# Kernel tuning notes

Measured on AMD Instinct MI355X. Metric: run time of the kernel, lower is better.

The kernel has to match this reference:

```python
import jax, jax.numpy as jnp
import numpy as np

B, S, H, NH, L = 2, 1024, 512, 8, 4
HD = H // NH
MLP = 4 * H
OUT = 128
SPARSITY = 0.8
EPS = 1e-5


def _pos_encoding(seq_len, d_model):
    pos = jnp.arange(seq_len, dtype=jnp.float32)[:, None]                     # [S,1]
    div = jnp.exp(jnp.arange(0, d_model, 2, dtype=jnp.float32) * (-np.log(10000.0) / d_model))
    ang = pos * div                                                            # [S,D/2]
    pe = jnp.stack([jnp.sin(ang), jnp.cos(ang)], axis=-1).reshape(seq_len, d_model)
    return pe[None]                                                            # [1,S,D]


def _layer_norm(x, g, b):
    m = jnp.mean(x, axis=-1, keepdims=True)
    v = jnp.mean(jnp.square(x - m), axis=-1, keepdims=True)
    return (x - m) * jax.lax.rsqrt(v + EPS) * g + b


def setup_inputs() -> dict:
    key = jax.random.key(0)
    ks = iter(jax.random.split(key, 16))
    w = lambda k, shp: jax.random.normal(k, shp, dtype=jnp.float32) * 0.02
    inp = {
        "x": jax.random.normal(next(ks), (B, S), dtype=jnp.float32),
        "in_w": w(next(ks), (1, H)), "in_b": jnp.zeros((H,), jnp.float32),
        "ln1_g": jnp.ones((L, H), jnp.float32), "ln1_b": jnp.zeros((L, H), jnp.float32),
        "qw": w(next(ks), (L, H, H)), "qb": jnp.zeros((L, H), jnp.float32),
        "kw": w(next(ks), (L, H, H)), "kb": jnp.zeros((L, H), jnp.float32),
        "vw": w(next(ks), (L, H, H)), "vb": jnp.zeros((L, H), jnp.float32),
        "ow": w(next(ks), (L, H, H)), "ob": jnp.zeros((L, H), jnp.float32),
        "ln2_g": jnp.ones((L, H), jnp.float32), "ln2_b": jnp.zeros((L, H), jnp.float32),
        "w1": w(next(ks), (L, H, MLP)), "b1": jnp.zeros((L, MLP), jnp.float32),
        "w2": w(next(ks), (L, MLP, H)), "b2": jnp.zeros((L, H), jnp.float32),
        "fn_g": jnp.ones((H,), jnp.float32), "fn_b": jnp.zeros((H,), jnp.float32),
        "out_w": w(next(ks), (H, OUT)), "out_b": jnp.zeros((OUT,), jnp.float32),
    }
    return inp


def _forward(x, in_w, in_b, ln1_g, ln1_b, qw, qb, kw, kb, vw, vb, ow, ob,
             ln2_g, ln2_b, w1, b1, w2, b2, fn_g, fn_b, out_w, out_b):
    seq_len = x.shape[1]
    k_top = max(1, int(seq_len * (1.0 - SPARSITY)))  # static
    scale = HD ** -0.5

    h = x[..., None] @ in_w + in_b                    # [B,S,H] (input_proj on [B,S,1])
    h = h + _pos_encoding(seq_len, H)

    layer_params = (ln1_g, ln1_b, qw, qb, kw, kb, vw, vb, ow, ob,
                    ln2_g, ln2_b, w1, b1, w2, b2)

    def block(h, p):
        (g1, bb1, Wq, bq, Wk, bk, Wv, bv, Wo, bo, g2, bb2, W1, B1, W2, B2) = p
        n = _layer_norm(h, g1, bb1)
        # project and split heads: [B,S,H] -> [B,NH,S,HD]
        def heads(W, b):
            y = n @ W + b
            return y.reshape(B, seq_len, NH, HD).transpose(0, 2, 1, 3)
        q, k, v = heads(Wq, bq), heads(Wk, bk), heads(Wv, bv)
        scores = jnp.einsum('bhqd,bhkd->bhqk', q, k) * scale
        # top-k sparsification: keep entries >= k-th largest per row (-inf elsewhere)
        kth = jax.lax.top_k(scores, k_top)[0][..., -1:]
        sparse = jnp.where(scores >= kth, scores, -jnp.inf)
        attn = jax.nn.softmax(sparse, axis=-1)
        o = jnp.einsum('bhqk,bhkd->bhqd', attn, v)
        o = o.transpose(0, 2, 1, 3).reshape(B, seq_len, H)
        h = h + (o @ Wo + bo)
        m = _layer_norm(h, g2, bb2)
        m = jax.nn.gelu(m @ W1 + B1, approximate=False) @ W2 + B2
        return h + m, attn

    h, attn_stack = jax.lax.scan(block, h, layer_params)
    out = _layer_norm(h, fn_g, fn_b) @ out_w + out_b  # [B,S,OUT]
    return out, attn_stack                            # attn_stack: [L,B,NH,S,S]


def reference(x, in_w, in_b, ln1_g, ln1_b, qw, qb, kw, kb, vw, vb, ow, ob,
              ln2_g, ln2_b, w1, b1, w2, b2, fn_g, fn_b, out_w, out_b):
    return _forward(x, in_w, in_b, ln1_g, ln1_b, qw, qb, kw, kb, vw, vb, ow, ob,
                    ln2_g, ln2_b, w1, b1, w2, b2, fn_g, fn_b, out_w, out_b)
```

## Files before the change

### kernel.cpp

```cpp
#include <hip/hip_runtime.h>
#include <math.h>

#define DEVINL __device__ __forceinline__

constexpr int S_   = 1024;
constexpr int H_   = 512;
constexpr int NH_  = 8;
constexpr int L_   = 4;
constexpr int HD_  = 64;
constexpr int MLP_ = 2048;
constexpr int OUT_ = 128;
constexpr int B_   = 2;
constexpr int BS_  = 2048;
constexpr int KTOP_ = 204;

typedef __bf16 bf16x8 __attribute__((ext_vector_type(8)));
typedef float f32x4 __attribute__((ext_vector_type(4)));

DEVINL unsigned short f2b(float f) {
  unsigned int u = __float_as_uint(f);
  unsigned int r = (u + 0x7fffu + ((u >> 16) & 1u)) >> 16;
  return (unsigned short)r;
}

DEVINL void gload16(const unsigned short* g, unsigned short* l) {
  __builtin_amdgcn_global_load_lds(
      (const __attribute__((address_space(1))) unsigned int*)g,
      (__attribute__((address_space(3))) unsigned int*)l,
      16, 0, 0);
}

__global__ __launch_bounds__(256) void transpose_conv_kernel(
    const float* __restrict__ src, unsigned short* __restrict__ dst, int R, int C)
{
  __shared__ float tile[32][33];
  const size_t base = (size_t)blockIdx.z * R * C;
  src += base; dst += base;
  const int c0 = blockIdx.x * 32;
  const int r0 = blockIdx.y * 32;
  const int tx = threadIdx.x & 31;
  const int ty = threadIdx.x >> 5;
#pragma unroll
  for (int j = 0; j < 4; j++)
    tile[ty + j * 8][tx] = src[(size_t)(r0 + ty + j * 8) * C + c0 + tx];
  __syncthreads();
#pragma unroll
  for (int j = 0; j < 4; j++)
    dst[(size_t)(c0 + ty + j * 8) * R + r0 + tx] = f2b(tile[tx][ty + j * 8]);
}

__global__ __launch_bounds__(256) void transpose_qkvo_kernel(
    const float* __restrict__ qw, const float* __restrict__ kw,
    const float* __restrict__ vw, const float* __restrict__ ow,
    unsigned short* __restrict__ qkv, unsigned short* __restrict__ ot)
{
  __shared__ float tile[32][33];
  const int z = blockIdx.z;
  const int which = z >> 2, l = z & 3;
  const float* src = (which == 0 ? qw : which == 1 ? kw : which == 2 ? vw : ow)
                     + (size_t)l * 512 * 512;
  unsigned short* dst = (which < 3)
      ? (qkv + (size_t)l * 1536 * 512 + (size_t)which * 512 * 512)
      : (ot + (size_t)l * 512 * 512);
  const int c0 = blockIdx.x * 32;
  const int r0 = blockIdx.y * 32;
  const int tx = threadIdx.x & 31;
  const int ty = threadIdx.x >> 5;
#pragma unroll
  for (int j = 0; j < 4; j++)
    tile[ty + j * 8][tx] = src[(size_t)(r0 + ty + j * 8) * 512 + c0 + tx];
  __syncthreads();
#pragma unroll
  for (int j = 0; j < 4; j++)
    dst[(size_t)(c0 + ty + j * 8) * 512 + r0 + tx] = f2b(tile[tx][ty + j * 8]);
}

__global__ __launch_bounds__(128) void input_pe_kernel(
    const float* __restrict__ x, const float* __restrict__ in_w,
    const float* __restrict__ in_b, float* __restrict__ h)
{
  const int row = blockIdx.x;
  const int s = row & (S_ - 1);
  const int c = threadIdx.x * 4;
  const float xv = x[row];
  const float4 wv = *(const float4*)(in_w + c);
  const float4 bv = *(const float4*)(in_b + c);
  const float* wp = (const float*)&wv;
  const float* bp = (const float*)&bv;
  float o[4];
#pragma unroll
  for (int j = 0; j < 4; j++) {
    const int cc = c + j;
    const float di = expf(-(float)(cc & ~1) * (9.210340371976184f / 512.0f));
    const float ang = (float)s * di;
    const float pe = (cc & 1) ? cosf(ang) : sinf(ang);
    o[j] = xv * wp[j] + bp[j] + pe;
  }
  *(float4*)(h + (size_t)row * H_ + c) = make_float4(o[0], o[1], o[2], o[3]);
}

__global__ __launch_bounds__(128) void ln_kernel(
    const float* __restrict__ hin, const float* __restrict__ g,
    const float* __restrict__ b, unsigned short* __restrict__ nout)
{
  const int row = blockIdx.x;
  const int t = threadIdx.x;
  const int wid = t >> 6, ln_ = t & 63;
  __shared__ float red[2];
  float4 v = ((const float4*)(hin + (size_t)row * H_))[t];
  float sm = v.x + v.y + v.z + v.w;
#pragma unroll
  for (int m = 1; m < 64; m <<= 1) sm += __shfl_xor(sm, m);
  if (ln_ == 0) red[wid] = sm;
  __syncthreads();
  const float mean = (red[0] + red[1]) * (1.0f / 512.0f);
  __syncthreads();
  const float dx = v.x - mean, dy = v.y - mean, dz = v.z - mean, dw = v.w - mean;
  float ss = dx * dx + dy * dy + dz * dz + dw * dw;
#pragma unroll
  for (int m = 1; m < 64; m <<= 1) ss += __shfl_xor(ss, m);
  if (ln_ == 0) red[wid] = ss;
  __syncthreads();
  const float var = (red[0] + red[1]) * (1.0f / 512.0f);
  const float rs = rsqrtf(var + 1e-5f);
  const float4 gv = ((const float4*)g)[t];
  const float4 bv = ((const float4*)b)[t];
  ushort4 o;
  o.x = f2b(dx * rs * gv.x + bv.x);
  o.y = f2b(dy * rs * gv.y + bv.y);
  o.z = f2b(dz * rs * gv.z + bv.z);
  o.w = f2b(dw * rs * gv.w + bv.w);
  ((ushort4*)(nout + (size_t)row * H_))[t] = o;
}

template <int EPI>
__global__ __launch_bounds__(256, 2) void gemm_kernel(
    const unsigned short* __restrict__ A, const unsigned short* __restrict__ Bt,
    const float* __restrict__ bias, void* __restrict__ Cout,
    int M, int N, int Klen, int Kstride,
    const float* __restrict__ bias2, const float* __restrict__ bias3,
    void* __restrict__ C2, void* __restrict__ C3)
{
  __shared__ unsigned short Alds[128 * 32];
  __shared__ unsigned short Blds[128 * 32];
  const int tid = threadIdx.x;
  const int w = tid >> 6, lane = tid & 63, lr = lane & 15, lg = lane >> 4;
  const int m0 = blockIdx.x * 128, n0 = blockIdx.y * 128;
  const int wm = (w >> 1) * 64, wn = (w & 1) * 64;

  A  += (size_t)blockIdx.z * Klen;
  Bt += (size_t)blockIdx.z * Klen;

  const int srow = w * 32 + (lane >> 2);
  const int scol = (lane & 3) * 8;
  const unsigned short* Ag0 = A + (size_t)(m0 + srow) * Kstride + scol;
  const unsigned short* Ag1 = A + (size_t)(m0 + srow + 16) * Kstride + scol;
  const unsigned short* Bg0 = Bt + (size_t)(n0 + srow) * Kstride + scol;
  const unsigned short* Bg1 = Bt + (size_t)(n0 + srow + 16) * Kstride + scol;
  unsigned short* Al0 = Alds + (w * 32) * 32;
  unsigned short* Al1 = Alds + (w * 32 + 16) * 32;
  unsigned short* Bl0 = Blds + (w * 32) * 32;
  unsigned short* Bl1 = Blds + (w * 32 + 16) * 32;

  const f32x4 zero4 = {0.f, 0.f, 0.f, 0.f};
  f32x4 acc[4][4];
#pragma unroll
  for (int i = 0; i < 4; i++)
#pragma unroll
    for (int j = 0; j < 4; j++) acc[i][j] = zero4;

  for (int kt = 0; kt < Klen; kt += 32) {
    __syncthreads();
    gload16(Ag0 + kt, Al0);
    gload16(Ag1 + kt, Al1);
    gload16(Bg0 + kt, Bl0);
    gload16(Bg1 + kt, Bl1);
    __syncthreads();
    bf16x8 af[4], bfr[4];
#pragma unroll
    for (int mi = 0; mi < 4; mi++)
      af[mi] = *(const bf16x8*)(Alds + (wm + mi * 16 + lr) * 32 + lg * 8);
#pragma unroll
    for (int ni = 0; ni < 4; ni++)
      bfr[ni] = *(const bf16x8*)(Blds + (wn + ni * 16 + lr) * 32 + lg * 8);
#pragma unroll
    for (int mi = 0; mi < 4; mi++)
#pragma unroll
      for (int ni = 0; ni < 4; ni++)
        acc[mi][ni] = __builtin_amdgcn_mfma_f32_16x16x32_bf16(af[mi], bfr[ni], acc[mi][ni], 0, 0, 0);
  }

#pragma unroll
  for (int mi = 0; mi < 4; mi++) {
#pragma unroll
    for (int ni = 0; ni < 4; ni++) {
      const int col = n0 + wn + ni * 16 + lr;
      if constexpr (EPI == 5) {
        if (col < 512) {
          const float bs = bias[col];
#pragma unroll
          for (int r = 0; r < 4; r++) {
            const int row = m0 + wm + mi * 16 + lg * 4 + r;
            ((unsigned short*)Cout)[(size_t)row * 512 + col] =
                f2b((acc[mi][ni][r] + bs) * 0.125f);
          }
        } else if (col < 1024) {
          const float bs = bias2[col - 512];
#pragma unroll
          for (int r = 0; r < 4; r++) {
            const int row = m0 + wm + mi * 16 + lg * 4 + r;
            ((unsigned short*)C2)[(size_t)row * 512 + (col - 512)] =
                f2b(acc[mi][ni][r] + bs);
          }
        } else {
          const float bs = bias3[col - 1024];
          const int row0_ = m0 + wm + mi * 16 + lg * 4;
          const int bb = row0_ >> 10, ssi = row0_ & 1023;
          ushort4 pk;
          pk.x = f2b(acc[mi][ni][0] + bs);
          pk.y = f2b(acc[mi][ni][1] + bs);
          pk.z = f2b(acc[mi][ni][2] + bs);
          pk.w = f2b(acc[mi][ni][3] + bs);
          *(ushort4*)((unsigned short*)C3 + ((size_t)(bb * 512 + (col - 1024))) * 1024 + ssi) = pk;
        }
      } else if constexpr (EPI == 6) {
        const float bs = (blockIdx.z == 0) ? bias[col] : 0.f;
#pragma unroll
        for (int r = 0; r < 4; r++) {
          const int row = m0 + wm + mi * 16 + lg * 4 + r;
          atomicAdd(&((float*)Cout)[(size_t)row * N + col], acc[mi][ni][r] + bs);
        }
      } else {
        const float bs = bias[col];
#pragma unroll
        for (int r = 0; r < 4; r++) {
          const int row = m0 + wm + mi * 16 + lg * 4 + r;
          float val = acc[mi][ni][r] + bs;
          const size_t idx = (size_t)row * N + col;
          if constexpr (EPI == 2) {
            val = 0.5f * val * (1.0f + erff(val * 0.7071067811865475f));
            ((unsigned short*)Cout)[idx] = f2b(val);
          } else {
            ((float*)Cout)[idx] = val;
          }
        }
      }
    }
  }
}

__global__ __launch_bounds__(256, 2) void attn_fused_kernel(
    const unsigned short* __restrict__ qbf, const unsigned short* __restrict__ kbf,
    const unsigned short* __restrict__ vt, float* __restrict__ attnL,
    unsigned short* __restrict__ obf)
{
  constexpr int LDF = 1032;
  __shared__ float sc[16 * LDF];
  const int mblk = blockIdx.x, bnh = blockIdx.y;
  const int b = bnh >> 3, nh = bnh & 7;
  const int tid = threadIdx.x, w = tid >> 6, lane = tid & 63;
  const int lr = lane & 15, lg = lane >> 4;
  const int row0 = mblk * 16;

  const unsigned short* qbase = qbf + ((size_t)(b * S_ + row0)) * H_ + nh * HD_;
  const unsigned short* kbase = kbf + (size_t)(b * S_) * H_ + nh * HD_;

  const f32x4 zero4 = {0.f, 0.f, 0.f, 0.f};

  {
    f32x4 acc[16];
#pragma unroll
    for (int kt = 0; kt < 16; kt++) acc[kt] = zero4;
    bf16x8 qf[2];
    qf[0] = *(const bf16x8*)(qbase + (size_t)lr * H_ + lg * 8);
    qf[1] = *(const bf16x8*)(qbase + (size_t)lr * H_ + 32 + lg * 8);
    const int kw0 = w * 256;
#pragma unroll
    for (int kt = 0; kt < 16; kt++) {
      const unsigned short* kp = kbase + (size_t)(kw0 + kt * 16 + lr) * H_ + lg * 8;
      const bf16x8 kf0 = *(const bf16x8*)(kp);
      const bf16x8 kf1 = *(const bf16x8*)(kp + 32);
      acc[kt] = __builtin_amdgcn_mfma_f32_16x16x32_bf16(kf0, qf[0], acc[kt], 0, 0, 0);
      acc[kt] = __builtin_amdgcn_mfma_f32_16x16x32_bf16(kf1, qf[1], acc[kt], 0, 0, 0);
    }
#pragma unroll
    for (int kt = 0; kt < 16; kt++)
      *(f32x4*)(sc + (size_t)lr * LDF + kw0 + kt * 16 + lg * 4) = acc[kt];
  }
  __syncthreads();

#pragma unroll 1
  for (int rr = 0; rr < 4; rr++) {
    const int row = w * 4 + rr;
    float* rowp = sc + (size_t)row * LDF;
    float v[16];
#pragma unroll
    for (int j = 0; j < 8; j++) {
      const float2 t2 = *(const float2*)(rowp + 2 * lane + j * 128);
      v[2 * j] = t2.x; v[2 * j + 1] = t2.y;
    }
    unsigned int keys[16];
#pragma unroll
    for (int j = 0; j < 16; j++) {
      const unsigned int u = __float_as_uint(v[j]);
      keys[j] = (u & 0x80000000u) ? ~u : (u | 0x80000000u);
    }
    unsigned int prefix = 0u;
#pragma unroll 1
    for (int bit = 31; bit >= 0; bit--) {
      const unsigned int cand = prefix | (1u << bit);
      int cnt = 0;
#pragma unroll
      for (int j = 0; j < 16; j++)
        cnt += (int)__popcll(__ballot(keys[j] >= cand));
      if (cnt >= KTOP_) prefix = cand;
    }
    const unsigned int fb = (prefix & 0x80000000u) ? (prefix & 0x7fffffffu) : ~prefix;
    const float thresh = __uint_as_float(fb);

    float mx = v[0];
#pragma unroll
    for (int j = 1; j < 16; j++) mx = fmaxf(mx, v[j]);
#pragma unroll
    for (int m = 1; m < 64; m <<= 1) mx = fmaxf(mx, __shfl_xor(mx, m));
    float p[16];
    float ssum = 0.f;
#pragma unroll
    for (int j = 0; j < 16; j++) {
      const float e = expf(v[j] - mx);
      p[j] = (v[j] >= thresh) ? e : 0.f;
      ssum += p[j];
    }
#pragma unroll
    for (int m = 1; m < 64; m <<= 1) ssum += __shfl_xor(ssum, m);
    const float inv = 1.0f / ssum;
    float* outrow = attnL + (size_t)bnh * S_ * S_ + (size_t)(row0 + row) * S_;
    unsigned short* prow = (unsigned short*)rowp;
#pragma unroll
    for (int j = 0; j < 8; j++) {
      const float p0 = p[2 * j] * inv, p1 = p[2 * j + 1] * inv;
      *(float2*)(outrow + 2 * lane + j * 128) = make_float2(p0, p1);
      const unsigned int pk = ((unsigned int)f2b(p1) << 16) | (unsigned int)f2b(p0);
      *(unsigned int*)(prow + 2 * lane + j * 128) = pk;
    }
  }
  __syncthreads();

  const unsigned short* vb = vt + (size_t)(b * 512 + nh * HD_) * S_;
  f32x4 oacc[4];
#pragma unroll
  for (int ni = 0; ni < 4; ni++) oacc[ni] = zero4;
  const unsigned short* scu = (const unsigned short*)sc;
#pragma unroll
  for (int ks = 0; ks < 8; ks++) {
    const int k0 = w * 256 + ks * 32;
    const bf16x8 pf = *(const bf16x8*)(scu + (size_t)lr * (2 * LDF) + k0 + lg * 8);
    bf16x8 vfr[4];
#pragma unroll
    for (int ni = 0; ni < 4; ni++)
      vfr[ni] = *(const bf16x8*)(vb + (size_t)(ni * 16 + lr) * S_ + k0 + lg * 8);
#pragma unroll
    for (int ni = 0; ni < 4; ni++)
      oacc[ni] = __builtin_amdgcn_mfma_f32_16x16x32_bf16(pf, vfr[ni], oacc[ni], 0, 0, 0);
  }
  __syncthreads();
  float* red = sc + w * 1024;
#pragma unroll
  for (int ni = 0; ni < 4; ni++)
#pragma unroll
    for (int r = 0; r < 4; r++)
      red[(lg * 4 + r) * 64 + ni * 16 + lr] = oacc[ni][r];
  __syncthreads();
  {
    const int orow = tid >> 4, oc0 = (tid & 15) * 4;
    const float* rp = sc + orow * 64 + oc0;
    float4 s0 = *(const float4*)rp;
#pragma unroll
    for (int ww = 1; ww < 4; ww++) {
      const float4 a = *(const float4*)(rp + ww * 1024);
      s0.x += a.x; s0.y += a.y; s0.z += a.z; s0.w += a.w;
    }
    ushort4 o1;
    o1.x = f2b(s0.x); o1.y = f2b(s0.y); o1.z = f2b(s0.z); o1.w = f2b(s0.w);
    unsigned short* dst = obf + (size_t)(b * S_ + row0 + orow) * H_ + nh * HD_ + oc0;
    *(ushort4*)dst = o1;
  }
}

extern "C" void kernel_launch(void* const* d_in, const int* in_sizes, int n_in,
                              void* d_out, int out_size, void* d_ws, size_t ws_size,
                              hipStream_t stream)
{
  (void)in_sizes; (void)n_in; (void)out_size; (void)ws_size;
  const float* x     = (const float*)d_in[0];
  const float* in_w  = (const float*)d_in[1];
  const float* in_b  = (const float*)d_in[2];
  const float* ln1_g = (const float*)d_in[3];
  const float* ln1_b = (const float*)d_in[4];
  const float* qw    = (const float*)d_in[5];
  const float* qbias = (const float*)d_in[6];
  const float* kw    = (const float*)d_in[7];
  const float* kbias = (const float*)d_in[8];
  const float* vw    = (const float*)d_in[9];
  const float* vbias = (const float*)d_in[10];
  const float* ow    = (const float*)d_in[11];
  const float* obias = (const float*)d_in[12];
  const float* ln2_g = (const float*)d_in[13];
  const float* ln2_b = (const float*)d_in[14];
  const float* w1    = (const float*)d_in[15];
  const float* b1    = (const float*)d_in[16];
  const float* w2    = (const float*)d_in[17];
  const float* b2    = (const float*)d_in[18];
  const float* fn_g  = (const float*)d_in[19];
  const float* fn_b  = (const float*)d_in[20];
  const float* out_w = (const float*)d_in[21];
  const float* out_b = (const float*)d_in[22];

  char* ws = (char*)d_ws;
  size_t off = 0;
  auto alloc = [&](size_t bytes) -> void* {
    void* p = ws + off;
    off += (bytes + 255) & ~(size_t)255;
    return p;
  };
  float* h             = (float*)alloc((size_t)BS_ * H_ * 4);
  unsigned short* Wqkvt = (unsigned short*)alloc((size_t)L_ * 1536 * H_ * 2);
  unsigned short* Wot  = (unsigned short*)alloc((size_t)L_ * H_ * H_ * 2);
  unsigned short* W1t  = (unsigned short*)alloc((size_t)L_ * MLP_ * H_ * 2);
  unsigned short* W2t  = (unsigned short*)alloc((size_t)L_ * H_ * MLP_ * 2);
  unsigned short* OWt  = (unsigned short*)alloc((size_t)OUT_ * H_ * 2);
  unsigned short* nbf  = (unsigned short*)alloc((size_t)BS_ * H_ * 2);
  unsigned short* qbf  = (unsigned short*)alloc((size_t)BS_ * H_ * 2);
  unsigned short* kbf  = (unsigned short*)alloc((size_t)BS_ * H_ * 2);
  unsigned short* vtb  = (unsigned short*)alloc((size_t)B_ * 512 * S_ * 2);
  unsigned short* obf  = (unsigned short*)alloc((size_t)BS_ * H_ * 2);
  unsigned short* tbf  = (unsigned short*)alloc((size_t)BS_ * MLP_ * 2);

  float* attn_base = (float*)d_out + (size_t)BS_ * OUT_;

  const dim3 tb(256);
  transpose_qkvo_kernel<<<dim3(16, 16, 16), tb, 0, stream>>>(qw, kw, vw, ow, Wqkvt, Wot);
  transpose_conv_kernel<<<dim3(64, 16, 4), tb, 0, stream>>>(w1, W1t, H_, MLP_);
  transpose_conv_kernel<<<dim3(16, 64, 4), tb, 0, stream>>>(w2, W2t, MLP_, H_);
  transpose_conv_kernel<<<dim3(4, 16, 1),  tb, 0, stream>>>(out_w, OWt, H_, OUT_);

  input_pe_kernel<<<dim3(BS_), dim3(128), 0, stream>>>(x, in_w, in_b, h);

  for (int l = 0; l < L_; l++) {
    float* attnL = attn_base + (size_t)l * 16 * S_ * S_;
    ln_kernel<<<dim3(BS_), dim3(128), 0, stream>>>(h, ln1_g + l * H_, ln1_b + l * H_, nbf);
    gemm_kernel<5><<<dim3(16, 12), tb, 0, stream>>>(
        nbf, Wqkvt + (size_t)l * 1536 * H_, qbias + l * H_, qbf, BS_, 1536, H_, H_,
        kbias + l * H_, vbias + l * H_, kbf, vtb);
    attn_fused_kernel<<<dim3(64, 16), tb, 0, stream>>>(qbf, kbf, vtb, attnL, obf);
    gemm_kernel<6><<<dim3(16, 4, 2), tb, 0, stream>>>(
        obf, Wot + (size_t)l * H_ * H_, obias + l * H_, h, BS_, H_, 256, H_,
        nullptr, nullptr, nullptr, nullptr);
    ln_kernel<<<dim3(BS_), dim3(128), 0, stream>>>(h, ln2_g + l * H_, ln2_b + l * H_, nbf);
    gemm_kernel<2><<<dim3(16, 16), tb, 0, stream>>>(
        nbf, W1t + (size_t)l * MLP_ * H_, b1 + l * MLP_, tbf, BS_, MLP_, H_, H_,
        nullptr, nullptr, nullptr, nullptr);
    gemm_kernel<6><<<dim3(16, 4, 4), tb, 0, stream>>>(
        tbf, W2t + (size_t)l * H_ * MLP_, b2 + l * H_, h, BS_, H_, 512, MLP_,
        nullptr, nullptr, nullptr, nullptr);
  }

  ln_kernel<<<dim3(BS_), dim3(128), 0, stream>>>(h, fn_g, fn_b, nbf);
  gemm_kernel<3><<<dim3(16, 1), tb, 0, stream>>>(
      nbf, OWt, out_b, d_out, BS_, OUT_, H_, H_,
      nullptr, nullptr, nullptr, nullptr);
}
```

Measured before the change: 1.037 ms.

## Double-buffer GEMM LDS tiles and merge prep kernels into one launch

The GEMM main loop now uses two LDS buffers, so the global-to-LDS load of the next K tile is issued before the MFMAs on the current tile, and each iteration needs one barrier instead of two. The four weight transpose/convert kernels and the input projection plus positional-encoding kernel are merged into a single prep launch that dispatches by block index. This targets load latency exposed inside the GEMM loop and per-launch overhead in setup. Double buffering doubles GEMM LDS use, which may reduce occupancy under launch_bounds(256,2).

New measurement: 1.035 ms. About the same (-0.2%).

```diff
diff --git a/kernel.cpp b/kernel.cpp
--- a/kernel.cpp
+++ b/kernel.cpp
@@ -30,16 +30,68 @@
       16, 0, 0);
 }
 
-__global__ __launch_bounds__(256) void transpose_conv_kernel(
-    const float* __restrict__ src, unsigned short* __restrict__ dst, int R, int C)
+__global__ __launch_bounds__(256) void prep_kernel(
+    const float* __restrict__ qw, const float* __restrict__ kw,
+    const float* __restrict__ vw, const float* __restrict__ ow,
+    const float* __restrict__ w1, const float* __restrict__ w2,
+    const float* __restrict__ outw,
+    const float* __restrict__ x, const float* __restrict__ in_w,
+    const float* __restrict__ in_b,
+    unsigned short* __restrict__ Wqkvt, unsigned short* __restrict__ Wot,
+    unsigned short* __restrict__ W1t, unsigned short* __restrict__ W2t,
+    unsigned short* __restrict__ OWt, float* __restrict__ h)
 {
+  const int bid = blockIdx.x;
+  if (bid >= 12352) {
+    const int idx = bid - 12352;
+    const int row = idx * 2 + (threadIdx.x >> 7);
+    const int s = row & (S_ - 1);
+    const int c = (threadIdx.x & 127) * 4;
+    const float xv = x[row];
+    const float4 wv = *(const float4*)(in_w + c);
+    const float4 bv = *(const float4*)(in_b + c);
+    const float* wp = (const float*)&wv;
+    const float* bp = (const float*)&bv;
+    float o[4];
+#pragma unroll
+    for (int j = 0; j < 4; j++) {
+      const int cc = c + j;
+      const float di = expf(-(float)(cc & ~1) * (9.210340371976184f / 512.0f));
+      const float ang = (float)s * di;
+      const float pe = (cc & 1) ? cosf(ang) : sinf(ang);
+      o[j] = xv * wp[j] + bp[j] + pe;
+    }
+    *(float4*)(h + (size_t)row * H_ + c) = make_float4(o[0], o[1], o[2], o[3]);
+    return;
+  }
+  const float* src; unsigned short* dst; int R, C, cx, ry;
+  if (bid < 4096) {
+    const int z = bid >> 8, rem = bid & 255;
+    const int which = z >> 2, l = z & 3;
+    src = (which == 0 ? qw : which == 1 ? kw : which == 2 ? vw : ow)
+          + (size_t)l * 512 * 512;
+    dst = (which < 3)
+        ? (Wqkvt + (size_t)l * 1536 * 512 + (size_t)which * 512 * 512)
+        : (Wot + (size_t)l * 512 * 512);
+    R = 512; C = 512; cx = rem & 15; ry = rem >> 4;
+  } else if (bid < 8192) {
+    const int idx = bid - 4096, z = idx >> 10, rem = idx & 1023;
+    src = w1 + (size_t)z * 512 * 2048;
+    dst = W1t + (size_t)z * 2048 * 512;
+    R = 512; C = 2048; cx = rem & 63; ry = rem >> 6;
+  } else if (bid < 12288) {
+    const int idx = bid - 8192, z = idx >> 10, rem = idx & 1023;
+    src = w2 + (size_t)z * 2048 * 512;
+    dst = W2t + (size_t)z * 512 * 2048;
+    R = 2048; C = 512; cx = rem & 15; ry = rem >> 4;
+  } else {
+    const int idx = bid - 12288;
+    src = outw; dst = OWt;
+    R = 512; C = 128; cx = idx & 3; ry = idx >> 2;
+  }
   __shared__ float tile[32][33];
-  const size_t base = (size_t)blockIdx.z * R * C;
-  src += base; dst += base;
-  const int c0 = blockIdx.x * 32;
-  const int r0 = blockIdx.y * 32;
-  const int tx = threadIdx.x & 31;
-  const int ty = threadIdx.x >> 5;
+  const int c0 = cx * 32, r0 = ry * 32;
+  const int tx = threadIdx.x & 31, ty = threadIdx.x >> 5;
 #pragma unroll
   for (int j = 0; j < 4; j++)
     tile[ty + j * 8][tx] = src[(size_t)(r0 + ty + j * 8) * C + c0 + tx];
@@ -47,56 +99,6 @@
 #pragma unroll
   for (int j = 0; j < 4; j++)
     dst[(size_t)(c0 + ty + j * 8) * R + r0 + tx] = f2b(tile[tx][ty + j * 8]);
-}
-
-__global__ __launch_bounds__(256) void transpose_qkvo_kernel(
-    const float* __restrict__ qw, const float* __restrict__ kw,
-    const float* __restrict__ vw, const float* __restrict__ ow,
-    unsigned short* __restrict__ qkv, unsigned short* __restrict__ ot)
-{
-  __shared__ float tile[32][33];
-  const int z = blockIdx.z;
-  const int which = z >> 2, l = z & 3;
-  const float* src = (which == 0 ? qw : which == 1 ? kw : which == 2 ? vw : ow)
-                     + (size_t)l * 512 * 512;
-  unsigned short* dst = (which < 3)
-      ? (qkv + (size_t)l * 1536 * 512 + (size_t)which * 512 * 512)
-      : (ot + (size_t)l * 512 * 512);
-  const int c0 = blockIdx.x * 32;
-  const int r0 = blockIdx.y * 32;
-  const int tx = threadIdx.x & 31;
-  const int ty = threadIdx.x >> 5;
-#pragma unroll
-  for (int j = 0; j < 4; j++)
-    tile[ty + j * 8][tx] = src[(size_t)(r0 + ty + j * 8) * 512 + c0 + tx];
-  __syncthreads();
-#pragma unroll
-  for (int j = 0; j < 4; j++)
-    dst[(size_t)(c0 + ty + j * 8) * 512 + r0 + tx] = f2b(tile[tx][ty + j * 8]);
-}
-
-__global__ __launch_bounds__(128) void input_pe_kernel(
-    const float* __restrict__ x, const float* __restrict__ in_w,
-    const float* __restrict__ in_b, float* __restrict__ h)
-{
-  const int row = blockIdx.x;
-  const int s = row & (S_ - 1);
-  const int c = threadIdx.x * 4;
-  const float xv = x[row];
-  const float4 wv = *(const float4*)(in_w + c);
-  const float4 bv = *(const float4*)(in_b + c);
-  const float* wp = (const float*)&wv;
-  const float* bp = (const float*)&bv;
-  float o[4];
-#pragma unroll
-  for (int j = 0; j < 4; j++) {
-    const int cc = c + j;
-    const float di = expf(-(float)(cc & ~1) * (9.210340371976184f / 512.0f));
-    const float ang = (float)s * di;
-    const float pe = (cc & 1) ? cosf(ang) : sinf(ang);
-    o[j] = xv * wp[j] + bp[j] + pe;
-  }
-  *(float4*)(h + (size_t)row * H_ + c) = make_float4(o[0], o[1], o[2], o[3]);
 }
 
 __global__ __launch_bounds__(128) void ln_kernel(
@@ -141,8 +143,8 @@
     const float* __restrict__ bias2, const float* __restrict__ bias3,
     void* __restrict__ C2, void* __restrict__ C3)
 {
-  __shared__ unsigned short Alds[128 * 32];
-  __shared__ unsigned short Blds[128 * 32];
+  __shared__ unsigned short Alds[2][128 * 32];
+  __shared__ unsigned short Blds[2][128 * 32];
   const int tid = threadIdx.x;
   const int w = tid >> 6, lane = tid & 63, lr = lane & 15, lg = lane >> 4;
   const int m0 = blockIdx.x * 128, n0 = blockIdx.y * 128;
@@ -157,10 +159,15 @@
   const unsigned short* Ag1 = A + (size_t)(m0 + srow + 16) * Kstride + scol;
   const unsigned short* Bg0 = Bt + (size_t)(n0 + srow) * Kstride + scol;
   const unsigned short* Bg1 = Bt + (size_t)(n0 + srow + 16) * Kstride + scol;
-  unsigned short* Al0 = Alds + (w * 32) * 32;
-  unsigned short* Al1 = Alds + (w * 32 + 16) * 32;
-  unsigned short* Bl0 = Blds + (w * 32) * 32;
-  unsigned short* Bl1 = Blds + (w * 32 + 16) * 32;
+  const int l0 = (w * 32) * 32;
+  const int l1 = (w * 32 + 16) * 32;
+
+  auto STAGE = [&](int buf, int kt) {
+    gload16(Ag0 + kt, &Alds[buf][l0]);
+    gload16(Ag1 + kt, &Alds[buf][l1]);
+    gload16(Bg0 + kt, &Blds[buf][l0]);
+    gload16(Bg1 + kt, &Blds[buf][l1]);
+  };
 
   const f32x4 zero4 = {0.f, 0.f, 0.f, 0.f};
   f32x4 acc[4][4];
@@ -169,25 +176,26 @@
 #pragma unroll
     for (int j = 0; j < 4; j++) acc[i][j] = zero4;
 
-  for (int kt = 0; kt < Klen; kt += 32) {
-    __syncthreads();
-    gload16(Ag0 + kt, Al0);
-    gload16(Ag1 + kt, Al1);
-    gload16(Bg0 + kt, Bl0);
-    gload16(Bg1 + kt, Bl1);
-    __syncthreads();
+  const int nsteps = Klen >> 5;
+  STAGE(0, 0);
+  __syncthreads();
+  int cur = 0;
+  for (int t = 0; t < nsteps; t++) {
+    if (t + 1 < nsteps) STAGE(cur ^ 1, (t + 1) * 32);
     bf16x8 af[4], bfr[4];
 #pragma unroll
     for (int mi = 0; mi < 4; mi++)
-      af[mi] = *(const bf16x8*)(Alds + (wm + mi * 16 + lr) * 32 + lg * 8);
+      af[mi] = *(const bf16x8*)(&Alds[cur][(wm + mi * 16 + lr) * 32 + lg * 8]);
 #pragma unroll
     for (int ni = 0; ni < 4; ni++)
-      bfr[ni] = *(const bf16x8*)(Blds + (wn + ni * 16 + lr) * 32 + lg * 8);
+      bfr[ni] = *(const bf16x8*)(&Blds[cur][(wn + ni * 16 + lr) * 32 + lg * 8]);
 #pragma unroll
     for (int mi = 0; mi < 4; mi++)
 #pragma unroll
       for (int ni = 0; ni < 4; ni++)
         acc[mi][ni] = __builtin_amdgcn_mfma_f32_16x16x32_bf16(af[mi], bfr[ni], acc[mi][ni], 0, 0, 0);
+    __syncthreads();
+    cur ^= 1;
   }
 
 #pragma unroll
@@ -439,12 +447,9 @@
   float* attn_base = (float*)d_out + (size_t)BS_ * OUT_;
 
   const dim3 tb(256);
-  transpose_qkvo_kernel<<<dim3(16, 16, 16), tb, 0, stream>>>(qw, kw, vw, ow, Wqkvt, Wot);
-  transpose_conv_kernel<<<dim3(64, 16, 4), tb, 0, stream>>>(w1, W1t, H_, MLP_);
-  transpose_conv_kernel<<<dim3(16, 64, 4), tb, 0, stream>>>(w2, W2t, MLP_, H_);
-  transpose_conv_kernel<<<dim3(4, 16, 1),  tb, 0, stream>>>(out_w, OWt, H_, OUT_);
-
-  input_pe_kernel<<<dim3(BS_), dim3(128), 0, stream>>>(x, in_w, in_b, h);
+  prep_kernel<<<dim3(13376), tb, 0, stream>>>(
+      qw, kw, vw, ow, w1, w2, out_w, x, in_w, in_b,
+      Wqkvt, Wot, W1t, W2t, OWt, h);
 
   for (int l = 0; l < L_; l++) {
     float* attnL = attn_base + (size_t)l * 16 * S_ * S_;
```
